# Performance work log

Measured on AMD Instinct MI355X. Metric: run time of the kernel, lower is better.

The kernel has to match this reference:

```python
import jax, jax.numpy as jnp
import numpy as np

NU, NI, D, B, L, E = 100000, 50000, 128, 3, 2, 1500000
N = NU + NI  # total nodes
EPS = 1e-5


def setup_inputs() -> dict:
    key = jax.random.key(0)
    ks = jax.random.split(key, 20)
    s = 0.05  # xavier-ish scale for 128-dim layers
    inp = {}
    inp["edge_index"] = jax.random.randint(ks[0], (2, E), 0, N, dtype=jnp.int32)
    inp["edge_type"] = jax.random.randint(ks[1], (E,), 0, B, dtype=jnp.int32)
    inp["item_feats"] = jax.random.normal(ks[2], (NI, D), jnp.float32)
    inp["user_emb"] = jax.random.normal(ks[3], (NU, D), jnp.float32) * s
    inp["user_proj_W"] = jax.random.normal(ks[4], (D, D), jnp.float32) * s
    inp["user_proj_b"] = jnp.zeros((D,), jnp.float32)
    inp["item_proj_W"] = jax.random.normal(ks[5], (D, D), jnp.float32) * s
    inp["item_proj_b"] = jnp.zeros((D,), jnp.float32)
    # stacked SAGEConv params: lin_l (neighbor, with bias) and lin_r (root, no bias)
    inp["sage_Wl"] = jax.random.normal(ks[6], (B, L, D, D), jnp.float32) * s
    inp["sage_bl"] = jnp.zeros((B, L, D), jnp.float32)
    inp["sage_Wr"] = jax.random.normal(ks[7], (B, L, D, D), jnp.float32) * s
    inp["bn_gamma"] = jnp.ones((B, L, D), jnp.float32)
    inp["bn_beta"] = jnp.zeros((B, L, D), jnp.float32)
    inp["query_W"] = jax.random.normal(ks[8], (D, D), jnp.float32) * s
    inp["query_b"] = jnp.zeros((D,), jnp.float32)
    inp["key_W"] = jax.random.normal(ks[9], (B, D, D), jnp.float32) * s
    inp["key_b"] = jnp.zeros((B, D), jnp.float32)
    inp["fuse_W"] = jax.random.normal(ks[10], (D, D), jnp.float32) * s
    inp["fuse_b"] = jnp.zeros((D,), jnp.float32)
    inp["refine_W"] = jax.random.normal(ks[11], (D, D), jnp.float32) * s
    inp["refine_b"] = jnp.zeros((D,), jnp.float32)
    return inp


def reference(edge_index, edge_type, item_feats, user_emb,
              user_proj_W, user_proj_b, item_proj_W, item_proj_b,
              sage_Wl, sage_bl, sage_Wr, bn_gamma, bn_beta,
              query_W, query_b, key_W, key_b,
              fuse_W, fuse_b, refine_W, refine_b):
    # initial node features: projected user embeddings + projected item feats
    x = jnp.concatenate([user_emb @ user_proj_W + user_proj_b,
                         item_feats @ item_proj_W + item_proj_b], axis=0)  # [N, D]
    src, dst = edge_index[0], edge_index[1]
    outs = []
    for b in range(B):
        # redirect edges of other behaviours to a dummy segment N (dropped)
        dst_b = jnp.where(edge_type == b, dst, N)
        cnt = jax.ops.segment_sum(jnp.ones((E,), x.dtype), dst_b, num_segments=N + 1)[:N]
        denom = jnp.maximum(cnt, 1.0)[:, None]
        h = x
        for l in range(L):
            # SAGEConv: mean-aggregate neighbor messages + root transform
            agg = jax.ops.segment_sum(h[src], dst_b, num_segments=N + 1)[:N] / denom
            h = agg @ sage_Wl[b, l] + sage_bl[b, l] + h @ sage_Wr[b, l]
            # BatchNorm1d (training-mode batch statistics, biased variance)
            mu = h.mean(axis=0)
            var = h.var(axis=0)
            h = (h - mu) * jax.lax.rsqrt(var + EPS) * bn_gamma[b, l] + bn_beta[b, l]
            if l < L - 1:
                h = jax.nn.relu(h)
        outs.append(x + h)  # residual
    stack = jnp.stack(outs, axis=0)  # [B, N, D]
    # attention fusion across behaviours
    Q = x @ query_W + query_b                                   # [N, D]
    K = jnp.einsum('bnd,bde->bne', stack, key_W) + key_b[:, None, :]  # [B, N, D]
    logits = jnp.einsum('nd,bnd->nb', Q, K)                      # [N, B]
    w = jax.nn.softmax(logits, axis=-1)
    fused = jnp.einsum('nb,bnd->nd', w, stack)
    fused = fused @ fuse_W + fuse_b
    # refine: Linear + ReLU (dropout is identity in eval)
    return jax.nn.relu(fused @ refine_W + refine_b)
```

## Files before the change

### kernel.cpp

```cpp
#include <hip/hip_runtime.h>

#define NUSER 100000
#define NITEM 50000
#define NNODE 150000
#define DIM 128
#define NB 3
#define NL 2
#define BN_EPS 1e-5f
#define NT3P 450560
#define SCAN_BLOCKS 440
#define TILESN 2344
#define BNABLK 9375

typedef unsigned short u16;
typedef _Float16 f16;
typedef __attribute__((ext_vector_type(8))) _Float16 f16x8;
typedef __attribute__((ext_vector_type(8))) unsigned short us8;
typedef __attribute__((ext_vector_type(4))) float f32x4;

__device__ __forceinline__ float h2f(u16 u) { f16 h; __builtin_memcpy(&h, &u, 2); return (float)h; }
__device__ __forceinline__ u16 f2h(float f) { f16 h = (f16)f; u16 u; __builtin_memcpy(&u, &h, 2); return u; }

struct Out3 { u16* p[3]; };
struct WPtrs { const float* s[8]; };


__global__ __launch_bounds__(256) void count_edges(const int* __restrict__ ei,
                                                   const int* __restrict__ et, int E,
                                                   int* __restrict__ cnt) {
    int t = blockIdx.x * 256 + threadIdx.x;
    if (t >= E) return;
    atomicAdd(&cnt[et[t] * NNODE + ei[E + t]], 1);
}

__global__ __launch_bounds__(256) void scan1(const int* __restrict__ cnt, int* __restrict__ bsum) {
    __shared__ int sh[256];
    int tid = threadIdx.x;
    int base = blockIdx.x * 1024 + tid * 4;
    int4 v = *(const int4*)(cnt + base);
    sh[tid] = v.x + v.y + v.z + v.w;
    __syncthreads();
    for (int off = 128; off > 0; off >>= 1) {
        if (tid < off) sh[tid] += sh[tid + off];
        __syncthreads();
    }
    if (tid == 0) bsum[blockIdx.x] = sh[0];
}

__global__ __launch_bounds__(512) void scan2(int* __restrict__ bsum, int nb) {
    __shared__ int sh[512];
    int tid = threadIdx.x;
    sh[tid] = (tid < nb) ? bsum[tid] : 0;
    __syncthreads();
    for (int off = 1; off < 512; off <<= 1) {
        int v = sh[tid];
        int add = (tid >= off) ? sh[tid - off] : 0;
        __syncthreads();
        sh[tid] = v + add;
        __syncthreads();
    }
    if (tid < nb) bsum[tid] = (tid == 0) ? 0 : sh[tid - 1];
}

__global__ __launch_bounds__(256) void scan3(const int* __restrict__ cnt, const int* __restrict__ bsum,
                                             int* __restrict__ row_start, int* __restrict__ cur) {
    __shared__ int sh[256];
    int tid = threadIdx.x;
    int base = blockIdx.x * 1024 + tid * 4;
    int4 v = *(const int4*)(cnt + base);
    sh[tid] = v.x + v.y + v.z + v.w;
    __syncthreads();
    for (int off = 1; off < 256; off <<= 1) {
        int a = sh[tid];
        int add = (tid >= off) ? sh[tid - off] : 0;
        __syncthreads();
        sh[tid] = a + add;
        __syncthreads();
    }
    int excl = ((tid == 0) ? 0 : sh[tid - 1]) + bsum[blockIdx.x];
    int4 o;
    o.x = excl; o.y = excl + v.x; o.z = o.y + v.y; o.w = o.z + v.z;
    *(int4*)(row_start + base) = o;
    *(int4*)(cur + base) = o;
}

__global__ __launch_bounds__(256) void scatter_csr(const int* __restrict__ ei,
                                                   const int* __restrict__ et, int E,
                                                   int* __restrict__ cur, int* __restrict__ adj) {
    int t = blockIdx.x * 256 + threadIdx.x;
    if (t >= E) return;
    int pos = atomicAdd(&cur[et[t] * NNODE + ei[E + t]], 1);
    adj[pos] = ei[t];
}


__global__ __launch_bounds__(256) void wconv_all(WPtrs w, u16* __restrict__ dst) {
    int gid = blockIdx.x * 256 + threadIdx.x;
    if (gid >= 20 * 16384) return;
    int m = gid >> 14, idx = gid & 16383;
    int k = idx & 127, n = idx >> 7;
    const float* src; int li;
    if (m == 0)       { src = w.s[0]; li = 0; }
    else if (m == 1)  { src = w.s[1]; li = 0; }
    else if (m < 8)   { src = w.s[2]; li = m - 2; }
    else if (m < 14)  { src = w.s[3]; li = m - 8; }
    else if (m == 14) { src = w.s[4]; li = 0; }
    else if (m < 18)  { src = w.s[5]; li = m - 15; }
    else if (m == 18) { src = w.s[6]; li = 0; }
    else              { src = w.s[7]; li = 0; }
    dst[(size_t)m * 16384 + idx] = f2h(src[(size_t)li * 16384 + k * 128 + n]);
}


__global__ __launch_bounds__(256) void bn_apply(u16* __restrict__ h,
                                                const float* __restrict__ stats6,
                                                const float* __restrict__ gamma,
                                                const float* __restrict__ beta) {
    __shared__ float sc[DIM];
    __shared__ float sf[DIM];
    const int tid = threadIdx.x;
    const int b = blockIdx.x / BNABLK;
    const int blk = blockIdx.x % BNABLK;
    const int bl = b * NL;
    if (tid < DIM) {
        const float* st = stats6 + bl * 256;
        const float invN = 1.0f / (float)NNODE;
        float mu = st[tid] * invN;
        float var = fmaxf(st[DIM + tid] * invN - mu * mu, 0.f);
        float scv = gamma[bl * DIM + tid] * rsqrtf(var + BN_EPS);
        sc[tid] = scv;
        sf[tid] = beta[bl * DIM + tid] - mu * scv;
    }
    __syncthreads();
    const int i = blk * 256 + tid;
    const int c8 = (i & 15) * 8;
    u16* p = h + (size_t)b * NNODE * DIM + (size_t)i * 8;
    us8 u = *(const us8*)p;
    us8 o;
#pragma unroll
    for (int j = 0; j < 8; ++j)
        o[j] = f2h(fmaxf(h2f(u[j]) * sc[c8 + j] + sf[c8 + j], 0.f));
    *(us8*)p = o;
}


__global__ __launch_bounds__(256, 4) void sage_layer(
    const u16* __restrict__ hin0, const u16* __restrict__ wt_Wl,
    const u16* __restrict__ wt_Wr, const float* __restrict__ sage_bl,
    float* __restrict__ stats6, Out3 outs, int layer,
    const int* __restrict__ adj, const int* __restrict__ row_start,
    const int* __restrict__ cnt) {
    __shared__ u16 T1[64][136];
    __shared__ float sstat[256];
    const int tid = threadIdx.x;
    const int b = blockIdx.x / TILESN;
    const int tile = blockIdx.x % TILESN;
    const int r0 = tile * 64;
    const int bl = b * NL + layer;
    const u16* hin = hin0 + (layer ? (size_t)b * NNODE * DIM : 0);
    const u16* Wl = wt_Wl + (size_t)bl * 16384;
    const u16* Wr = wt_Wr + (size_t)bl * 16384;

    sstat[tid] = 0.f;

    {
        const int row = tid >> 2;
        const int c0 = (tid & 3) * 32;
        float a[32];
#pragma unroll
        for (int j = 0; j < 32; ++j) a[j] = 0.f;
        const int n = r0 + row;
        if (n < NNODE) {
            const int base = b * NNODE + n;
            const int s0 = row_start[base];
            const int deg = cnt[base];
            int e = 0;
            for (; e + 3 < deg; e += 4) {
                const int i0 = adj[s0 + e],     i1 = adj[s0 + e + 1];
                const int i2 = adj[s0 + e + 2], i3 = adj[s0 + e + 3];
                const u16* p0 = hin + (size_t)i0 * DIM + c0;
                const u16* p1 = hin + (size_t)i1 * DIM + c0;
                const u16* p2 = hin + (size_t)i2 * DIM + c0;
                const u16* p3 = hin + (size_t)i3 * DIM + c0;
                us8 u00 = *(const us8*)p0,        u01 = *(const us8*)(p0 + 8);
                us8 u02 = *(const us8*)(p0 + 16), u03 = *(const us8*)(p0 + 24);
                us8 u10 = *(const us8*)p1,        u11 = *(const us8*)(p1 + 8);
                us8 u12 = *(const us8*)(p1 + 16), u13 = *(const us8*)(p1 + 24);
                us8 u20 = *(const us8*)p2,        u21 = *(const us8*)(p2 + 8);
                us8 u22 = *(const us8*)(p2 + 16), u23 = *(const us8*)(p2 + 24);
                us8 u30 = *(const us8*)p3,        u31 = *(const us8*)(p3 + 8);
                us8 u32 = *(const us8*)(p3 + 16), u33 = *(const us8*)(p3 + 24);
#pragma unroll
                for (int j = 0; j < 8; ++j) {
                    a[j]      += (h2f(u00[j]) + h2f(u10[j])) + (h2f(u20[j]) + h2f(u30[j]));
                    a[8 + j]  += (h2f(u01[j]) + h2f(u11[j])) + (h2f(u21[j]) + h2f(u31[j]));
                    a[16 + j] += (h2f(u02[j]) + h2f(u12[j])) + (h2f(u22[j]) + h2f(u32[j]));
                    a[24 + j] += (h2f(u03[j]) + h2f(u13[j])) + (h2f(u23[j]) + h2f(u33[j]));
                }
            }
            if (e + 1 < deg) {
                const u16* p1 = hin + (size_t)adj[s0 + e] * DIM + c0;
                const u16* p2 = hin + (size_t)adj[s0 + e + 1] * DIM + c0;
                us8 u0 = *(const us8*)p1,        u1 = *(const us8*)(p1 + 8);
                us8 u2 = *(const us8*)(p1 + 16), u3 = *(const us8*)(p1 + 24);
                us8 v0 = *(const us8*)p2,        v1 = *(const us8*)(p2 + 8);
                us8 v2 = *(const us8*)(p2 + 16), v3 = *(const us8*)(p2 + 24);
#pragma unroll
                for (int j = 0; j < 8; ++j) {
                    a[j]      += h2f(u0[j]) + h2f(v0[j]);
                    a[8 + j]  += h2f(u1[j]) + h2f(v1[j]);
                    a[16 + j] += h2f(u2[j]) + h2f(v2[j]);
                    a[24 + j] += h2f(u3[j]) + h2f(v3[j]);
                }
                e += 2;
            }
            if (e < deg) {
                const u16* p1 = hin + (size_t)adj[s0 + e] * DIM + c0;
                us8 u0 = *(const us8*)p1,        u1 = *(const us8*)(p1 + 8);
                us8 u2 = *(const us8*)(p1 + 16), u3 = *(const us8*)(p1 + 24);
#pragma unroll
                for (int j = 0; j < 8; ++j) {
                    a[j]      += h2f(u0[j]);
                    a[8 + j]  += h2f(u1[j]);
                    a[16 + j] += h2f(u2[j]);
                    a[24 + j] += h2f(u3[j]);
                }
            }
            const float s = 1.0f / (float)(deg > 1 ? deg : 1);
#pragma unroll
            for (int j = 0; j < 32; ++j) a[j] *= s;
        }
#pragma unroll
        for (int k = 0; k < 4; ++k) {
            us8 o;
#pragma unroll
            for (int j = 0; j < 8; ++j) o[j] = f2h(a[8 * k + j]);
            *(us8*)&T1[row][c0 + 8 * k] = o;
        }
    }
    __syncthreads();

    const int wave = tid >> 6, lane = tid & 63, q = lane >> 4, rlo = lane & 15;
    const f16x8 zf = (f16x8)(f16)0.f;
    f32x4 acc[4][2];
#pragma unroll
    for (int t = 0; t < 4; ++t) { acc[t][0] = (f32x4)0.f; acc[t][1] = (f32x4)0.f; }
#pragma unroll
    for (int kc = 0; kc < DIM; kc += 32) {
        f16x8 b1v[2], b2v[2];
#pragma unroll
        for (int c = 0; c < 2; ++c) {
            b1v[c] = *(const f16x8*)(Wl + (size_t)(wave * 32 + 16 * c + rlo) * DIM + kc + q * 8);
            b2v[c] = *(const f16x8*)(Wr + (size_t)(wave * 32 + 16 * c + rlo) * DIM + kc + q * 8);
        }
#pragma unroll
        for (int t = 0; t < 4; ++t) {
            f16x8 a1 = *(const f16x8*)&T1[16 * t + rlo][kc + q * 8];
            int rr = r0 + 16 * t + rlo;
            f16x8 a2 = (rr < NNODE) ? *(const f16x8*)(hin + (size_t)rr * DIM + kc + q * 8) : zf;
            acc[t][0] = __builtin_amdgcn_mfma_f32_16x16x32_f16(a1, b1v[0], acc[t][0], 0, 0, 0);
            acc[t][1] = __builtin_amdgcn_mfma_f32_16x16x32_f16(a1, b1v[1], acc[t][1], 0, 0, 0);
            acc[t][0] = __builtin_amdgcn_mfma_f32_16x16x32_f16(a2, b2v[0], acc[t][0], 0, 0, 0);
            acc[t][1] = __builtin_amdgcn_mfma_f32_16x16x32_f16(a2, b2v[1], acc[t][1], 0, 0, 0);
        }
    }

    const int col0 = wave * 32 + rlo, col1 = col0 + 16;
    const float bb0 = sage_bl[bl * DIM + col0], bb1 = sage_bl[bl * DIM + col1];
    const bool tiled = (layer == 1) && (b > 0);
    u16* Cb;
    if (!tiled) {
        Cb = outs.p[b];
    } else {
        Cb = ((tile == TILESN - 1) ? outs.p[2]
                                   : outs.p[1] + (size_t)tile * 16384)
             + (size_t)(b - 1) * 8192;
    }
    float rs0 = 0, rq0 = 0, rs1 = 0, rq1 = 0;
#pragma unroll
    for (int t = 0; t < 4; ++t) {
#pragma unroll
        for (int r = 0; r < 4; ++r) {
            int rloc = 16 * t + q * 4 + r;
            int row = r0 + rloc;
            if (row >= NNODE) continue;
            float v0 = acc[t][0][r] + bb0;
            float v1 = acc[t][1][r] + bb1;
            rs0 += v0; rq0 += v0 * v0; rs1 += v1; rq1 += v1 * v1;
            size_t off = tiled ? (size_t)rloc * DIM : (size_t)row * DIM;
            Cb[off + col0] = f2h(v0);
            Cb[off + col1] = f2h(v1);
        }
    }
    rs0 += __shfl_xor(rs0, 16); rs0 += __shfl_xor(rs0, 32);
    rq0 += __shfl_xor(rq0, 16); rq0 += __shfl_xor(rq0, 32);
    rs1 += __shfl_xor(rs1, 16); rs1 += __shfl_xor(rs1, 32);
    rq1 += __shfl_xor(rq1, 16); rq1 += __shfl_xor(rq1, 32);
    if (q == 0) {
        atomicAdd(&sstat[col0], rs0);
        atomicAdd(&sstat[DIM + col0], rq0);
        atomicAdd(&sstat[col1], rs1);
        atomicAdd(&sstat[DIM + col1], rq1);
    }
    __syncthreads();
    if (tid < DIM) {
        float* so = stats6 + bl * 256;
        atomicAdd(&so[tid], sstat[tid]);
        atomicAdd(&so[DIM + tid], sstat[DIM + tid]);
    }
}


__global__ __launch_bounds__(256) void attn_fuse(
    const u16* __restrict__ hpre0, const u16* __restrict__ hpre12,
    const u16* __restrict__ tailb, const float* __restrict__ stats6,
    const float* __restrict__ gamma, const float* __restrict__ beta,
    const u16* __restrict__ xh, const u16* __restrict__ wt,
    const float* __restrict__ query_b, const float* __restrict__ key_b,
    const float* __restrict__ fuse_b, const float* __restrict__ refine_b,
    float* __restrict__ out) {
    __shared__ __attribute__((aligned(16))) u16 St[3][64][136];
    __shared__ float sc[3][DIM], sf[3][DIM];
    __shared__ float slog[64][4];
    __shared__ float swt[64][4];
    const int tid = threadIdx.x;
    const int tile = blockIdx.x;
    const int r0 = tile * 64;
    const u16* wt_q    = wt + 14 * 16384;
    const u16* wt_key  = wt + 15 * 16384;
    const u16* wt_fuse = wt + 18 * 16384;
    const u16* wt_ref  = wt + 19 * 16384;

    if (tid < DIM) {
        const float invN = 1.0f / (float)NNODE;
#pragma unroll
        for (int b = 0; b < NB; ++b) {
            const int bl = b * NL + 1;
            const float* st = stats6 + bl * 256;
            float mu = st[tid] * invN;
            float var = fmaxf(st[DIM + tid] * invN - mu * mu, 0.f);
            float c = gamma[bl * DIM + tid] * rsqrtf(var + BN_EPS);
            sc[b][tid] = c;
            sf[b][tid] = beta[bl * DIM + tid] - mu * c;
        }
    }
    if (tid < 64) { slog[tid][0] = 0.f; slog[tid][1] = 0.f; slog[tid][2] = 0.f; }
    __syncthreads();

    for (int i = tid; i < 1024; i += 256) {
        int r = i >> 4, c8 = (i & 15) * 8;
        int n = r0 + r;
        if (n < NNODE) {
            us8 xv = *(const us8*)(xh + (size_t)n * DIM + c8);
#pragma unroll
            for (int b = 0; b < NB; ++b) {
                const u16* src = (b == 0)
                    ? hpre0 + (size_t)n * DIM + c8
                    : ((tile == TILESN - 1) ? tailb : hpre12 + (size_t)tile * 16384)
                      + (size_t)(b - 1) * 8192 + r * DIM + c8;
                us8 hv = *(const us8*)src;
                us8 o;
#pragma unroll
                for (int j = 0; j < 8; ++j)
                    o[j] = f2h(h2f(hv[j]) * sc[b][c8 + j] + sf[b][c8 + j] + h2f(xv[j]));
                *(us8*)&St[b][r][c8] = o;
            }
        } else {
            us8 z = (us8)(u16)0;
#pragma unroll
            for (int b = 0; b < NB; ++b) *(us8*)&St[b][r][c8] = z;
        }
    }
    __syncthreads();

    const int wave = tid >> 6, lane = tid & 63, q = lane >> 4, rlo = lane & 15;
    const int col0 = wave * 32 + rlo, col1 = col0 + 16;
    const f16x8 zf = (f16x8)(f16)0.f;

    f32x4 qa[4][2];
#pragma unroll
    for (int t = 0; t < 4; ++t) { qa[t][0] = (f32x4)0.f; qa[t][1] = (f32x4)0.f; }
#pragma unroll
    for (int kc = 0; kc < DIM; kc += 32) {
        f16x8 bv0 = *(const f16x8*)(wt_q + (size_t)(wave * 32 + rlo) * DIM + kc + q * 8);
        f16x8 bv1 = *(const f16x8*)(wt_q + (size_t)(wave * 32 + 16 + rlo) * DIM + kc + q * 8);
#pragma unroll
        for (int t = 0; t < 4; ++t) {
            int rr = r0 + 16 * t + rlo;
            f16x8 av = (rr < NNODE) ? *(const f16x8*)(xh + (size_t)rr * DIM + kc + q * 8) : zf;
            qa[t][0] = __builtin_amdgcn_mfma_f32_16x16x32_f16(av, bv0, qa[t][0], 0, 0, 0);
            qa[t][1] = __builtin_amdgcn_mfma_f32_16x16x32_f16(av, bv1, qa[t][1], 0, 0, 0);
        }
    }
    {
        const float qb0 = query_b[col0], qb1 = query_b[col1];
#pragma unroll
        for (int t = 0; t < 4; ++t)
#pragma unroll
            for (int r = 0; r < 4; ++r) { qa[t][0][r] += qb0; qa[t][1][r] += qb1; }
    }

#pragma unroll
    for (int b = 0; b < NB; ++b) {
        f32x4 ka[4][2];
#pragma unroll
        for (int t = 0; t < 4; ++t) { ka[t][0] = (f32x4)0.f; ka[t][1] = (f32x4)0.f; }
        const u16* Wk = wt_key + (size_t)b * 16384;
#pragma unroll
        for (int kc = 0; kc < DIM; kc += 32) {
            f16x8 bv0 = *(const f16x8*)(Wk + (size_t)(wave * 32 + rlo) * DIM + kc + q * 8);
            f16x8 bv1 = *(const f16x8*)(Wk + (size_t)(wave * 32 + 16 + rlo) * DIM + kc + q * 8);
#pragma unroll
            for (int t = 0; t < 4; ++t) {
                f16x8 av = *(const f16x8*)&St[b][16 * t + rlo][kc + q * 8];
                ka[t][0] = __builtin_amdgcn_mfma_f32_16x16x32_f16(av, bv0, ka[t][0], 0, 0, 0);
                ka[t][1] = __builtin_amdgcn_mfma_f32_16x16x32_f16(av, bv1, ka[t][1], 0, 0, 0);
            }
        }
        const float kb0 = key_b[b * DIM + col0], kb1 = key_b[b * DIM + col1];
#pragma unroll
        for (int t = 0; t < 4; ++t) {
#pragma unroll
            for (int r = 0; r < 4; ++r) {
                int rloc = 16 * t + q * 4 + r;
                float v = (ka[t][0][r] + kb0) * qa[t][0][r]
                        + (ka[t][1][r] + kb1) * qa[t][1][r];
                v += __shfl_xor(v, 1);
                v += __shfl_xor(v, 2);
                v += __shfl_xor(v, 4);
                v += __shfl_xor(v, 8);
                if (rlo == 0) atomicAdd(&slog[rloc][b], v);
            }
        }
    }
    __syncthreads();

    if (tid < 64) {
        float l0 = slog[tid][0], l1 = slog[tid][1], l2 = slog[tid][2];
        float mm = fmaxf(l0, fmaxf(l1, l2));
        float e0 = expf(l0 - mm), e1 = expf(l1 - mm), e2 = expf(l2 - mm);
        float inv = 1.0f / (e0 + e1 + e2);
        swt[tid][0] = e0 * inv; swt[tid][1] = e1 * inv; swt[tid][2] = e2 * inv;
    }
    __syncthreads();

    f32x4 facc[4][2];
#pragma unroll
    for (int t = 0; t < 4; ++t) { facc[t][0] = (f32x4)0.f; facc[t][1] = (f32x4)0.f; }
#pragma unroll
    for (int b = 0; b < NB; ++b) {
        f32x4 ga[4][2];
#pragma unroll
        for (int t = 0; t < 4; ++t) { ga[t][0] = (f32x4)0.f; ga[t][1] = (f32x4)0.f; }
#pragma unroll
        for (int kc = 0; kc < DIM; kc += 32) {
            f16x8 bv0 = *(const f16x8*)(wt_fuse + (size_t)(wave * 32 + rlo) * DIM + kc + q * 8);
            f16x8 bv1 = *(const f16x8*)(wt_fuse + (size_t)(wave * 32 + 16 + rlo) * DIM + kc + q * 8);
#pragma unroll
            for (int t = 0; t < 4; ++t) {
                f16x8 av = *(const f16x8*)&St[b][16 * t + rlo][kc + q * 8];
                ga[t][0] = __builtin_amdgcn_mfma_f32_16x16x32_f16(av, bv0, ga[t][0], 0, 0, 0);
                ga[t][1] = __builtin_amdgcn_mfma_f32_16x16x32_f16(av, bv1, ga[t][1], 0, 0, 0);
            }
        }
#pragma unroll
        for (int t = 0; t < 4; ++t) {
#pragma unroll
            for (int r = 0; r < 4; ++r) {
                int rloc = 16 * t + q * 4 + r;
                float wgt = swt[rloc][b];
                facc[t][0][r] += wgt * ga[t][0][r];
                facc[t][1][r] += wgt * ga[t][1][r];
            }
        }
    }
    __syncthreads();

    {
        const float fb0 = fuse_b[col0], fb1 = fuse_b[col1];
#pragma unroll
        for (int t = 0; t < 4; ++t) {
#pragma unroll
            for (int r = 0; r < 4; ++r) {
                int rloc = 16 * t + q * 4 + r;
                St[0][rloc][col0] = f2h(facc[t][0][r] + fb0);
                St[0][rloc][col1] = f2h(facc[t][1][r] + fb1);
            }
        }
    }
    __syncthreads();

    f32x4 racc[4][2];
#pragma unroll
    for (int t = 0; t < 4; ++t) { racc[t][0] = (f32x4)0.f; racc[t][1] = (f32x4)0.f; }
#pragma unroll
    for (int kc = 0; kc < DIM; kc += 32) {
        f16x8 bv0 = *(const f16x8*)(wt_ref + (size_t)(wave * 32 + rlo) * DIM + kc + q * 8);
        f16x8 bv1 = *(const f16x8*)(wt_ref + (size_t)(wave * 32 + 16 + rlo) * DIM + kc + q * 8);
#pragma unroll
        for (int t = 0; t < 4; ++t) {
            f16x8 av = *(const f16x8*)&St[0][16 * t + rlo][kc + q * 8];
            racc[t][0] = __builtin_amdgcn_mfma_f32_16x16x32_f16(av, bv0, racc[t][0], 0, 0, 0);
            racc[t][1] = __builtin_amdgcn_mfma_f32_16x16x32_f16(av, bv1, racc[t][1], 0, 0, 0);
        }
    }
    {
        const float rb0 = refine_b[col0], rb1 = refine_b[col1];
#pragma unroll
        for (int t = 0; t < 4; ++t) {
#pragma unroll
            for (int r = 0; r < 4; ++r) {
                int row = r0 + 16 * t + q * 4 + r;
                if (row >= NNODE) continue;
                out[(size_t)row * DIM + col0] = fmaxf(racc[t][0][r] + rb0, 0.f);
                out[(size_t)row * DIM + col1] = fmaxf(racc[t][1][r] + rb1, 0.f);
            }
        }
    }
}


__global__ __launch_bounds__(256) void gemm_p(
    const void* __restrict__ Av, const u16* __restrict__ Wt,
    const float* __restrict__ bias, void* __restrict__ Cv, int M, int flags) {
    const u16* A16 = (const u16*)Av;
    const float* A32 = (const float*)Av;
    const float* bs = bias;
    const int r0 = blockIdx.x * 64;
    const int tid = threadIdx.x;
    const int wave = tid >> 6, lane = tid & 63, q = lane >> 4, rlo = lane & 15;
    f32x4 acc[4][2];
#pragma unroll
    for (int t = 0; t < 4; ++t) { acc[t][0] = (f32x4)0.f; acc[t][1] = (f32x4)0.f; }
    const f16x8 zf = (f16x8)(f16)0.f;
#pragma unroll
    for (int kc = 0; kc < DIM; kc += 32) {
        f16x8 av[4], bv[2];
#pragma unroll
        for (int t = 0; t < 4; ++t) {
            int row = r0 + 16 * t + rlo;
            if (row < M) {
                if (flags & 8) {
                    const float* p = A32 + (size_t)row * DIM + kc + q * 8;
                    float4 x0 = *(const float4*)p;
                    float4 x1 = *(const float4*)(p + 4);
                    f16x8 tmp;
                    tmp[0] = (f16)x0.x; tmp[1] = (f16)x0.y; tmp[2] = (f16)x0.z; tmp[3] = (f16)x0.w;
                    tmp[4] = (f16)x1.x; tmp[5] = (f16)x1.y; tmp[6] = (f16)x1.z; tmp[7] = (f16)x1.w;
                    av[t] = tmp;
                } else {
                    av[t] = *(const f16x8*)(A16 + (size_t)row * DIM + kc + q * 8);
                }
            } else {
                av[t] = zf;
            }
        }
#pragma unroll
        for (int c = 0; c < 2; ++c)
            bv[c] = *(const f16x8*)(Wt + (size_t)(wave * 32 + 16 * c + rlo) * DIM + kc + q * 8);
#pragma unroll
        for (int t = 0; t < 4; ++t) {
            acc[t][0] = __builtin_amdgcn_mfma_f32_16x16x32_f16(av[t], bv[0], acc[t][0], 0, 0, 0);
            acc[t][1] = __builtin_amdgcn_mfma_f32_16x16x32_f16(av[t], bv[1], acc[t][1], 0, 0, 0);
        }
    }

    const int col0 = wave * 32 + rlo, col1 = col0 + 16;
    const float bb0 = bs[col0], bb1 = bs[col1];
#pragma unroll
    for (int t = 0; t < 4; ++t) {
#pragma unroll
        for (int r = 0; r < 4; ++r) {
            int row = r0 + 16 * t + q * 4 + r;
            if (row >= M) continue;
            float v0 = acc[t][0][r] + bb0;
            float v1 = acc[t][1][r] + bb1;
            if (flags & 1) { v0 = fmaxf(v0, 0.f); v1 = fmaxf(v1, 0.f); }
            if (flags & 32) {
                ((u16*)Cv)[(size_t)row * DIM + col0] = f2h(v0);
                ((u16*)Cv)[(size_t)row * DIM + col1] = f2h(v1);
            } else {
                ((float*)Cv)[(size_t)row * DIM + col0] = v0;
                ((float*)Cv)[(size_t)row * DIM + col1] = v1;
            }
        }
    }
}


extern "C" void kernel_launch(void* const* d_in, const int* in_sizes, int n_in,
                              void* d_out, int out_size, void* d_ws, size_t ws_size,
                              hipStream_t stream) {
    const int* edge_index    = (const int*)d_in[0];
    const int* edge_type     = (const int*)d_in[1];
    const float* item_feats  = (const float*)d_in[2];
    const float* user_emb    = (const float*)d_in[3];
    const float* user_proj_b = (const float*)d_in[5];
    const float* item_proj_b = (const float*)d_in[7];
    const float* sage_bl  = (const float*)d_in[9];
    const float* bn_gamma = (const float*)d_in[11];
    const float* bn_beta  = (const float*)d_in[12];
    const float* query_b  = (const float*)d_in[14];
    const float* key_b    = (const float*)d_in[16];
    const float* fuse_b   = (const float*)d_in[18];
    const float* refine_b = (const float*)d_in[20];
    const int E = in_sizes[1];

    const size_t ND = (size_t)NNODE * DIM;
    char* w = (char*)d_ws;
    u16* xh = (u16*)w;          w += ND * 2;
    u16* stackb = (u16*)w;      w += NB * ND * 2;
    u16* fbuf = (u16*)w;        w += ND * 2;
    int* cnt = (int*)w;         w += (size_t)NT3P * 4;
    int* row_start = (int*)w;   w += (size_t)NT3P * 4;
    int* cur = (int*)w;         w += (size_t)NT3P * 4;
    int* adj = (int*)w;         w += (size_t)E * 4;
    u16* wt = (u16*)w;          w += (size_t)20 * 16384 * 2;
    int* bsum = (int*)w;        w += 2048;
    float* stats6 = (float*)w;  w += 6 * 256 * 4;
    u16* tailb = (u16*)w;       w += 32768;

    const u16* wt_user = wt;
    const u16* wt_item = wt + 16384;
    const u16* wt_Wl   = wt + 2 * 16384;
    const u16* wt_Wr   = wt + 8 * 16384;

    u16* dout16 = (u16*)d_out;

    hipMemsetAsync(cnt, 0, (size_t)NT3P * 4, stream);
    hipMemsetAsync(stats6, 0, 6 * 256 * 4, stream);
    int gE = (E + 255) / 256;
    count_edges<<<gE, 256, 0, stream>>>(edge_index, edge_type, E, cnt);
    scan1<<<SCAN_BLOCKS, 256, 0, stream>>>(cnt, bsum);
    scan2<<<1, 512, 0, stream>>>(bsum, SCAN_BLOCKS);
    scan3<<<SCAN_BLOCKS, 256, 0, stream>>>(cnt, bsum, row_start, cur);
    scatter_csr<<<gE, 256, 0, stream>>>(edge_index, edge_type, E, cur, adj);

    WPtrs wp;
    wp.s[0] = (const float*)d_in[4];
    wp.s[1] = (const float*)d_in[6];
    wp.s[2] = (const float*)d_in[8];
    wp.s[3] = (const float*)d_in[10];
    wp.s[4] = (const float*)d_in[13];
    wp.s[5] = (const float*)d_in[15];
    wp.s[6] = (const float*)d_in[17];
    wp.s[7] = (const float*)d_in[19];
    wconv_all<<<1280, 256, 0, stream>>>(wp, wt);

    const int TU = (NUSER + 63) / 64, TI = (NITEM + 63) / 64;
    gemm_p<<<TU, 256, 0, stream>>>(user_emb, wt_user, user_proj_b, xh, NUSER, 8 | 32);
    gemm_p<<<TI, 256, 0, stream>>>(item_feats, wt_item, item_proj_b,
                                   xh + (size_t)NUSER * DIM, NITEM, 8 | 32);

    Out3 out_l0, out_l1;
    for (int b = 0; b < NB; ++b) out_l0.p[b] = stackb + (size_t)b * ND;
    out_l1.p[0] = fbuf;
    out_l1.p[1] = dout16;
    out_l1.p[2] = tailb;

    sage_layer<<<NB * TILESN, 256, 0, stream>>>(xh, wt_Wl, wt_Wr, sage_bl,
                                                stats6, out_l0, 0,
                                                adj, row_start, cnt);
    bn_apply<<<NB * BNABLK, 256, 0, stream>>>(stackb, stats6, bn_gamma, bn_beta);
    sage_layer<<<NB * TILESN, 256, 0, stream>>>(stackb, wt_Wl, wt_Wr, sage_bl,
                                                stats6, out_l1, 1,
                                                adj, row_start, cnt);

    attn_fuse<<<TILESN, 256, 0, stream>>>(fbuf, dout16, tailb, stats6,
                                          bn_gamma, bn_beta, xh, wt,
                                          query_b, key_b, fuse_b, refine_b,
                                          (float*)d_out);
}
```

Measured before the change: 1.009 ms.

## Shrink attention tile to 32 rows and raise sage_layer occupancy

```diff
diff --git a/kernel.cpp b/kernel.cpp
--- a/kernel.cpp
+++ b/kernel.cpp
@@ -10,6 +10,7 @@
 #define NT3P 450560
 #define SCAN_BLOCKS 440
 #define TILESN 2344
+#define NT32 4688
 #define BNABLK 9375
 
 typedef unsigned short u16;
@@ -144,7 +145,7 @@
 }
 
 
-__global__ __launch_bounds__(256, 4) void sage_layer(
+__global__ __launch_bounds__(256, 8) void sage_layer(
     const u16* __restrict__ hin0, const u16* __restrict__ wt_Wl,
     const u16* __restrict__ wt_Wr, const float* __restrict__ sage_bl,
     float* __restrict__ stats6, Out3 outs, int layer,
@@ -175,30 +176,7 @@
             const int s0 = row_start[base];
             const int deg = cnt[base];
             int e = 0;
-            for (; e + 3 < deg; e += 4) {
-                const int i0 = adj[s0 + e],     i1 = adj[s0 + e + 1];
-                const int i2 = adj[s0 + e + 2], i3 = adj[s0 + e + 3];
-                const u16* p0 = hin + (size_t)i0 * DIM + c0;
-                const u16* p1 = hin + (size_t)i1 * DIM + c0;
-                const u16* p2 = hin + (size_t)i2 * DIM + c0;
-                const u16* p3 = hin + (size_t)i3 * DIM + c0;
-                us8 u00 = *(const us8*)p0,        u01 = *(const us8*)(p0 + 8);
-                us8 u02 = *(const us8*)(p0 + 16), u03 = *(const us8*)(p0 + 24);
-                us8 u10 = *(const us8*)p1,        u11 = *(const us8*)(p1 + 8);
-                us8 u12 = *(const us8*)(p1 + 16), u13 = *(const us8*)(p1 + 24);
-                us8 u20 = *(const us8*)p2,        u21 = *(const us8*)(p2 + 8);
-                us8 u22 = *(const us8*)(p2 + 16), u23 = *(const us8*)(p2 + 24);
-                us8 u30 = *(const us8*)p3,        u31 = *(const us8*)(p3 + 8);
-                us8 u32 = *(const us8*)(p3 + 16), u33 = *(const us8*)(p3 + 24);
-#pragma unroll
-                for (int j = 0; j < 8; ++j) {
-                    a[j]      += (h2f(u00[j]) + h2f(u10[j])) + (h2f(u20[j]) + h2f(u30[j]));
-                    a[8 + j]  += (h2f(u01[j]) + h2f(u11[j])) + (h2f(u21[j]) + h2f(u31[j]));
-                    a[16 + j] += (h2f(u02[j]) + h2f(u12[j])) + (h2f(u22[j]) + h2f(u32[j]));
-                    a[24 + j] += (h2f(u03[j]) + h2f(u13[j])) + (h2f(u23[j]) + h2f(u33[j]));
-                }
-            }
-            if (e + 1 < deg) {
+            for (; e + 1 < deg; e += 2) {
                 const u16* p1 = hin + (size_t)adj[s0 + e] * DIM + c0;
                 const u16* p2 = hin + (size_t)adj[s0 + e + 1] * DIM + c0;
                 us8 u0 = *(const us8*)p1,        u1 = *(const us8*)(p1 + 8);
@@ -212,7 +190,6 @@
                     a[16 + j] += h2f(u2[j]) + h2f(v2[j]);
                     a[24 + j] += h2f(u3[j]) + h2f(v3[j]);
                 }
-                e += 2;
             }
             if (e < deg) {
                 const u16* p1 = hin + (size_t)adj[s0 + e] * DIM + c0;
@@ -268,14 +245,6 @@
     const int col0 = wave * 32 + rlo, col1 = col0 + 16;
     const float bb0 = sage_bl[bl * DIM + col0], bb1 = sage_bl[bl * DIM + col1];
     const bool tiled = (layer == 1) && (b > 0);
-    u16* Cb;
-    if (!tiled) {
-        Cb = outs.p[b];
-    } else {
-        Cb = ((tile == TILESN - 1) ? outs.p[2]
-                                   : outs.p[1] + (size_t)tile * 16384)
-             + (size_t)(b - 1) * 8192;
-    }
     float rs0 = 0, rq0 = 0, rs1 = 0, rq1 = 0;
 #pragma unroll
     for (int t = 0; t < 4; ++t) {
@@ -287,9 +256,18 @@
             float v0 = acc[t][0][r] + bb0;
             float v1 = acc[t][1][r] + bb1;
             rs0 += v0; rq0 += v0 * v0; rs1 += v1; rq1 += v1 * v1;
-            size_t off = tiled ? (size_t)rloc * DIM : (size_t)row * DIM;
-            Cb[off + col0] = f2h(v0);
-            Cb[off + col1] = f2h(v1);
+            if (!tiled) {
+                u16* C = outs.p[b];
+                C[(size_t)row * DIM + col0] = f2h(v0);
+                C[(size_t)row * DIM + col1] = f2h(v1);
+            } else {
+                int tt = row >> 5, rl = row & 31;
+                u16* base = (tt == NT32 - 1) ? outs.p[2]
+                                             : outs.p[1] + (size_t)tt * 8192;
+                base += (size_t)(b - 1) * 4096 + rl * DIM;
+                base[col0] = f2h(v0);
+                base[col1] = f2h(v1);
+            }
         }
     }
     rs0 += __shfl_xor(rs0, 16); rs0 += __shfl_xor(rs0, 32);
@@ -319,13 +297,13 @@
     const float* __restrict__ query_b, const float* __restrict__ key_b,
     const float* __restrict__ fuse_b, const float* __restrict__ refine_b,
     float* __restrict__ out) {
-    __shared__ __attribute__((aligned(16))) u16 St[3][64][136];
+    __shared__ __attribute__((aligned(16))) u16 St[3][32][136];
     __shared__ float sc[3][DIM], sf[3][DIM];
-    __shared__ float slog[64][4];
-    __shared__ float swt[64][4];
+    __shared__ float slog[32][4];
+    __shared__ float swt[32][4];
     const int tid = threadIdx.x;
     const int tile = blockIdx.x;
-    const int r0 = tile * 64;
+    const int r0 = tile * 32;
     const u16* wt_q    = wt + 14 * 16384;
     const u16* wt_key  = wt + 15 * 16384;
     const u16* wt_fuse = wt + 18 * 16384;
@@ -344,10 +322,10 @@
             sf[b][tid] = beta[bl * DIM + tid] - mu * c;
         }
     }
-    if (tid < 64) { slog[tid][0] = 0.f; slog[tid][1] = 0.f; slog[tid][2] = 0.f; }
-    __syncthreads();
-
-    for (int i = tid; i < 1024; i += 256) {
+    if (tid < 32) { slog[tid][0] = 0.f; slog[tid][1] = 0.f; slog[tid][2] = 0.f; }
+    __syncthreads();
+
+    for (int i = tid; i < 512; i += 256) {
         int r = i >> 4, c8 = (i & 15) * 8;
         int n = r0 + r;
         if (n < NNODE) {
@@ -356,8 +334,8 @@
             for (int b = 0; b < NB; ++b) {
                 const u16* src = (b == 0)
                     ? hpre0 + (size_t)n * DIM + c8
-                    : ((tile == TILESN - 1) ? tailb : hpre12 + (size_t)tile * 16384)
-                      + (size_t)(b - 1) * 8192 + r * DIM + c8;
+                    : ((tile == NT32 - 1) ? tailb : hpre12 + (size_t)tile * 8192)
+                      + (size_t)(b - 1) * 4096 + r * DIM + c8;
                 us8 hv = *(const us8*)src;
                 us8 o;
 #pragma unroll
@@ -377,15 +355,15 @@
     const int col0 = wave * 32 + rlo, col1 = col0 + 16;
     const f16x8 zf = (f16x8)(f16)0.f;
 
-    f32x4 qa[4][2];
-#pragma unroll
-    for (int t = 0; t < 4; ++t) { qa[t][0] = (f32x4)0.f; qa[t][1] = (f32x4)0.f; }
+    f32x4 qa[2][2];
+#pragma unroll
+    for (int t = 0; t < 2; ++t) { qa[t][0] = (f32x4)0.f; qa[t][1] = (f32x4)0.f; }
 #pragma unroll
     for (int kc = 0; kc < DIM; kc += 32) {
         f16x8 bv0 = *(const f16x8*)(wt_q + (size_t)(wave * 32 + rlo) * DIM + kc + q * 8);
         f16x8 bv1 = *(const f16x8*)(wt_q + (size_t)(wave * 32 + 16 + rlo) * DIM + kc + q * 8);
 #pragma unroll
-        for (int t = 0; t < 4; ++t) {
+        for (int t = 0; t < 2; ++t) {
             int rr = r0 + 16 * t + rlo;
             f16x8 av = (rr < NNODE) ? *(const f16x8*)(xh + (size_t)rr * DIM + kc + q * 8) : zf;
             qa[t][0] = __builtin_amdgcn_mfma_f32_16x16x32_f16(av, bv0, qa[t][0], 0, 0, 0);
@@ -395,23 +373,23 @@
     {
         const float qb0 = query_b[col0], qb1 = query_b[col1];
 #pragma unroll
-        for (int t = 0; t < 4; ++t)
+        for (int t = 0; t < 2; ++t)
 #pragma unroll
             for (int r = 0; r < 4; ++r) { qa[t][0][r] += qb0; qa[t][1][r] += qb1; }
     }
 
 #pragma unroll
     for (int b = 0; b < NB; ++b) {
-        f32x4 ka[4][2];
-#pragma unroll
-        for (int t = 0; t < 4; ++t) { ka[t][0] = (f32x4)0.f; ka[t][1] = (f32x4)0.f; }
+        f32x4 ka[2][2];
+#pragma unroll
+        for (int t = 0; t < 2; ++t) { ka[t][0] = (f32x4)0.f; ka[t][1] = (f32x4)0.f; }
         const u16* Wk = wt_key + (size_t)b * 16384;
 #pragma unroll
         for (int kc = 0; kc < DIM; kc += 32) {
             f16x8 bv0 = *(const f16x8*)(Wk + (size_t)(wave * 32 + rlo) * DIM + kc + q * 8);
             f16x8 bv1 = *(const f16x8*)(Wk + (size_t)(wave * 32 + 16 + rlo) * DIM + kc + q * 8);
 #pragma unroll
-            for (int t = 0; t < 4; ++t) {
+            for (int t = 0; t < 2; ++t) {
                 f16x8 av = *(const f16x8*)&St[b][16 * t + rlo][kc + q * 8];
                 ka[t][0] = __builtin_amdgcn_mfma_f32_16x16x32_f16(av, bv0, ka[t][0], 0, 0, 0);
                 ka[t][1] = __builtin_amdgcn_mfma_f32_16x16x32_f16(av, bv1, ka[t][1], 0, 0, 0);
@@ -419,7 +397,7 @@
         }
         const float kb0 = key_b[b * DIM + col0], kb1 = key_b[b * DIM + col1];
 #pragma unroll
-        for (int t = 0; t < 4; ++t) {
+        for (int t = 0; t < 2; ++t) {
 #pragma unroll
             for (int r = 0; r < 4; ++r) {
                 int rloc = 16 * t + q * 4 + r;
@@ -435,7 +413,7 @@
     }
     __syncthreads();
 
-    if (tid < 64) {
+    if (tid < 32) {
         float l0 = slog[tid][0], l1 = slog[tid][1], l2 = slog[tid][2];
         float mm = fmaxf(l0, fmaxf(l1, l2));
         float e0 = expf(l0 - mm), e1 = expf(l1 - mm), e2 = expf(l2 - mm);
@@ -444,27 +422,27 @@
     }
     __syncthreads();
 
-    f32x4 facc[4][2];
-#pragma unroll
-    for (int t = 0; t < 4; ++t) { facc[t][0] = (f32x4)0.f; facc[t][1] = (f32x4)0.f; }
+    f32x4 facc[2][2];
+#pragma unroll
+    for (int t = 0; t < 2; ++t) { facc[t][0] = (f32x4)0.f; facc[t][1] = (f32x4)0.f; }
 #pragma unroll
     for (int b = 0; b < NB; ++b) {
-        f32x4 ga[4][2];
-#pragma unroll
-        for (int t = 0; t < 4; ++t) { ga[t][0] = (f32x4)0.f; ga[t][1] = (f32x4)0.f; }
+        f32x4 ga[2][2];
+#pragma unroll
+        for (int t = 0; t < 2; ++t) { ga[t][0] = (f32x4)0.f; ga[t][1] = (f32x4)0.f; }
 #pragma unroll
         for (int kc = 0; kc < DIM; kc += 32) {
             f16x8 bv0 = *(const f16x8*)(wt_fuse + (size_t)(wave * 32 + rlo) * DIM + kc + q * 8);
             f16x8 bv1 = *(const f16x8*)(wt_fuse + (size_t)(wave * 32 + 16 + rlo) * DIM + kc + q * 8);
 #pragma unroll
-            for (int t = 0; t < 4; ++t) {
+            for (int t = 0; t < 2; ++t) {
                 f16x8 av = *(const f16x8*)&St[b][16 * t + rlo][kc + q * 8];
                 ga[t][0] = __builtin_amdgcn_mfma_f32_16x16x32_f16(av, bv0, ga[t][0], 0, 0, 0);
                 ga[t][1] = __builtin_amdgcn_mfma_f32_16x16x32_f16(av, bv1, ga[t][1], 0, 0, 0);
             }
         }
 #pragma unroll
-        for (int t = 0; t < 4; ++t) {
+        for (int t = 0; t < 2; ++t) {
 #pragma unroll
             for (int r = 0; r < 4; ++r) {
                 int rloc = 16 * t + q * 4 + r;
@@ -479,7 +457,7 @@
     {
         const float fb0 = fuse_b[col0], fb1 = fuse_b[col1];
 #pragma unroll
-        for (int t = 0; t < 4; ++t) {
+        for (int t = 0; t < 2; ++t) {
 #pragma unroll
             for (int r = 0; r < 4; ++r) {
                 int rloc = 16 * t + q * 4 + r;
@@ -490,15 +468,15 @@
     }
     __syncthreads();
 
-    f32x4 racc[4][2];
-#pragma unroll
-    for (int t = 0; t < 4; ++t) { racc[t][0] = (f32x4)0.f; racc[t][1] = (f32x4)0.f; }
+    f32x4 racc[2][2];
+#pragma unroll
+    for (int t = 0; t < 2; ++t) { racc[t][0] = (f32x4)0.f; racc[t][1] = (f32x4)0.f; }
 #pragma unroll
     for (int kc = 0; kc < DIM; kc += 32) {
         f16x8 bv0 = *(const f16x8*)(wt_ref + (size_t)(wave * 32 + rlo) * DIM + kc + q * 8);
         f16x8 bv1 = *(const f16x8*)(wt_ref + (size_t)(wave * 32 + 16 + rlo) * DIM + kc + q * 8);
 #pragma unroll
-        for (int t = 0; t < 4; ++t) {
+        for (int t = 0; t < 2; ++t) {
             f16x8 av = *(const f16x8*)&St[0][16 * t + rlo][kc + q * 8];
             racc[t][0] = __builtin_amdgcn_mfma_f32_16x16x32_f16(av, bv0, racc[t][0], 0, 0, 0);
             racc[t][1] = __builtin_amdgcn_mfma_f32_16x16x32_f16(av, bv1, racc[t][1], 0, 0, 0);
@@ -507,7 +485,7 @@
     {
         const float rb0 = refine_b[col0], rb1 = refine_b[col1];
 #pragma unroll
-        for (int t = 0; t < 4; ++t) {
+        for (int t = 0; t < 2; ++t) {
 #pragma unroll
             for (int r = 0; r < 4; ++r) {
                 int row = r0 + 16 * t + q * 4 + r;
@@ -618,7 +596,7 @@
     u16* wt = (u16*)w;          w += (size_t)20 * 16384 * 2;
     int* bsum = (int*)w;        w += 2048;
     float* stats6 = (float*)w;  w += 6 * 256 * 4;
-    u16* tailb = (u16*)w;       w += 32768;
+    u16* tailb = (u16*)w;       w += 16384;
 
     const u16* wt_user = wt;
     const u16* wt_item = wt + 16384;
@@ -666,8 +644,8 @@
                                                 stats6, out_l1, 1,
                                                 adj, row_start, cnt);
 
-    attn_fuse<<<TILESN, 256, 0, stream>>>(fbuf, dout16, tailb, stats6,
-                                          bn_gamma, bn_beta, xh, wt,
-                                          query_b, key_b, fuse_b, refine_b,
-                                          (float*)d_out);
-}
+    attn_fuse<<<NT32, 256, 0, stream>>>(fbuf, dout16, tailb, stats6,
+                                        bn_gamma, bn_beta, xh, wt,
+                                        query_b, key_b, fuse_b, refine_b,
+                                        (float*)d_out);
+}
```

After: 1.102 ms. +9.2%, slower.
